# Kernel tuning notes

Measured on AMD Instinct MI355X. Metric: run time of the kernel, lower is better.

## Reference

```python
import jax, jax.numpy as jnp
import numpy as np

H = 16      # num_attention_heads
D = 1024    # hidden_size
DH = D // H # attention_head_size
LN_EPS = 1e-5


def setup_inputs() -> dict:
    key = jax.random.key(0)
    ks = jax.random.split(key, 12)
    B, S = 2, 2048
    s = 0.02
    return {
        "hidden_states": jax.random.normal(ks[0], (B, S, D), jnp.float32),
        "attention_mask": jnp.zeros((B, 1, 1, S), jnp.float32),
        "Wq": jax.random.normal(ks[1], (D, D), jnp.float32) * s,
        "bq": jnp.zeros((D,), jnp.float32),
        "Wk": jax.random.normal(ks[2], (D, D), jnp.float32) * s,
        "bk": jnp.zeros((D,), jnp.float32),
        "Wv": jax.random.normal(ks[3], (D, D), jnp.float32) * s,
        "bv": jnp.zeros((D,), jnp.float32),
        "med_bias": jax.random.normal(ks[4], (H, 1, 1), jnp.float32) * s,
        "Wo": jax.random.normal(ks[5], (D, D), jnp.float32) * s,
        "bo": jnp.zeros((D,), jnp.float32),
        "gamma": jnp.ones((D,), jnp.float32),
        "beta": jnp.zeros((D,), jnp.float32),
    }


def _heads(x):
    # (B,S,D) -> (B,H,S,DH)
    B, S, _ = x.shape
    return x.reshape(B, S, H, DH).transpose(0, 2, 1, 3)


def reference(hidden_states, attention_mask, Wq, bq, Wk, bk, Wv, bv,
              med_bias, Wo, bo, gamma, beta):
    B, S, _ = hidden_states.shape
    q = _heads(hidden_states @ Wq.T + bq)
    k = _heads(hidden_states @ Wk.T + bk)
    v = _heads(hidden_states @ Wv.T + bv)

    scale = 1.0 / jnp.sqrt(jnp.asarray(DH, hidden_states.dtype))
    # scores: (B,H,S,S); per-head medical bias + additive mask
    scores = jnp.einsum('bhqd,bhkd->bhqk', q, k) * scale
    scores = scores + med_bias[None, :, :, :] + attention_mask
    probs = jax.nn.softmax(scores, axis=-1)  # dropout is identity in eval

    ctx = jnp.einsum('bhqk,bhkd->bhqd', probs, v)
    ctx = ctx.transpose(0, 2, 1, 3).reshape(B, S, D)

    attn_out = ctx @ Wo.T + bo
    x = hidden_states + attn_out

    mu = jnp.mean(x, axis=-1, keepdims=True)
    var = jnp.mean(jnp.square(x - mu), axis=-1, keepdims=True)
    return (x - mu) * jax.lax.rsqrt(var + LN_EPS) * gamma + beta
```

## Files before the change

kernel.cpp:

```cpp
#include <hip/hip_runtime.h>
#include <hip/hip_bf16.h>

#define S_LEN 2048
#define NH 16
#define DH 64
#define DMODEL 1024
#define M_TOT 4096
#define LOG2E 1.44269504f

typedef __attribute__((ext_vector_type(8))) short bf16x8;
typedef __attribute__((ext_vector_type(4))) float f32x4;
typedef unsigned short u16;
typedef unsigned short us8 __attribute__((ext_vector_type(8)));

__device__ inline u16 f2bf(float f) {
    union { float f; unsigned u; } c; c.f = f;
    unsigned r = c.u + 0x7fffu + ((c.u >> 16) & 1u);
    return (u16)(r >> 16);
}

__device__ inline void load_lds16(const u16* g, u16* l) {
    __builtin_amdgcn_global_load_lds((const __attribute__((address_space(1))) void*)g,
                                     (__attribute__((address_space(3))) void*)l, 16, 0, 0);
}

__device__ inline us8 pack8(float4 a, float4 b) {
    us8 o;
    o[0] = f2bf(a.x); o[1] = f2bf(a.y); o[2] = f2bf(a.z); o[3] = f2bf(a.w);
    o[4] = f2bf(b.x); o[5] = f2bf(b.y); o[6] = f2bf(b.z); o[7] = f2bf(b.w);
    return o;
}

__global__ __launch_bounds__(256) void conv_bf16(
    const float* __restrict__ src, u16* __restrict__ dst)
{
    const size_t i = ((size_t)blockIdx.x * 256 + threadIdx.x) * 8;
    const float4 a = *(const float4*)(src + i);
    const float4 b = *(const float4*)(src + i + 4);
    *(us8*)(dst + i) = pack8(a, b);
}

__global__ __launch_bounds__(256) void conv4(
    const float* __restrict__ w0, const float* __restrict__ w1,
    const float* __restrict__ w2, const float* __restrict__ w3,
    u16* __restrict__ dst)
{
    const int z = blockIdx.y;
    const float* src = (z == 0) ? w0 : (z == 1) ? w1 : (z == 2) ? w2 : w3;
    const size_t i = ((size_t)blockIdx.x * 256 + threadIdx.x) * 8;
    const float4 a = *(const float4*)(src + i);
    const float4 b = *(const float4*)(src + i + 4);
    *(us8*)(dst + (size_t)z * (DMODEL * DMODEL) + i) = pack8(a, b);
}

__global__ __launch_bounds__(256) void gen_cm(
    const float* __restrict__ mask, float* __restrict__ cm, u16* __restrict__ cmb)
{
    const int i = blockIdx.x * 256 + threadIdx.x;
    const float c = exp2f(mask[i] * LOG2E);
    cm[i] = c;
    cmb[i] = f2bf(c);
}

__global__ __launch_bounds__(256) void gemm_qkv(
    const u16* __restrict__ hsb, const u16* __restrict__ wbf,
    const float* __restrict__ bq, const float* __restrict__ bk, const float* __restrict__ bv,
    const float* __restrict__ cm,
    u16* __restrict__ qb, u16* __restrict__ kb, u16* __restrict__ vT)
{
    __shared__ u16 lA[2][128 * 32];
    __shared__ u16 lB[2][128 * 32];
    const int tid = threadIdx.x, lane = tid & 63, w = tid >> 6;
    const int l15 = lane & 15, lg = lane >> 4;
    const int wr = w >> 1, wc = w & 1;
    const int m0 = blockIdx.y * 128, n0 = blockIdx.x * 128;
    const int z = blockIdx.z;
    const u16* Wp = wbf + (size_t)z * (DMODEL * DMODEL);
    const float* bias = (z == 0) ? bq : (z == 1) ? bk : bv;

    const u16 *aptr[2], *wptr[2]; int adst[2];
#pragma unroll
    for (int i = 0; i < 2; ++i) {
        const int rowb = (w * 2 + i) * 16;
        const int row = rowb + (lane >> 2);
        const int gc = (lane & 3) ^ ((row >> 1) & 3);
        aptr[i] = hsb + (size_t)(m0 + row) * DMODEL + gc * 8;
        wptr[i] = Wp + (size_t)(n0 + row) * DMODEL + gc * 8;
        adst[i] = rowb * 32;
    }
    int afo[4], bfo[4];
#pragma unroll
    for (int i = 0; i < 4; ++i) {
        const int rA = wr * 64 + i * 16 + l15;
        afo[i] = rA * 32 + ((lg ^ ((rA >> 1) & 3)) * 8);
        const int rB = wc * 64 + i * 16 + l15;
        bfo[i] = rB * 32 + ((lg ^ ((rB >> 1) & 3)) * 8);
    }

    f32x4 acc[4][4] = {};

#pragma unroll
    for (int i = 0; i < 2; ++i) {
        load_lds16(aptr[i], &lA[0][adst[i]]);
        load_lds16(wptr[i], &lB[0][adst[i]]);
    }

    int cur = 0;
    for (int t = 0; t < 32; ++t) {
        if (t < 31) {
#pragma unroll
            for (int i = 0; i < 2; ++i) {
                load_lds16(aptr[i] + (t + 1) * 32, &lA[cur ^ 1][adst[i]]);
                load_lds16(wptr[i] + (t + 1) * 32, &lB[cur ^ 1][adst[i]]);
            }
            asm volatile("s_waitcnt vmcnt(4)" ::: "memory");
        } else {
            asm volatile("s_waitcnt vmcnt(0)" ::: "memory");
        }
        __builtin_amdgcn_s_barrier();
        __builtin_amdgcn_sched_barrier(0);

        bf16x8 af[4], bfr[4];
#pragma unroll
        for (int i = 0; i < 4; ++i) {
            af[i] = *(bf16x8*)&lA[cur][afo[i]];
            bfr[i] = *(bf16x8*)&lB[cur][bfo[i]];
        }
        __builtin_amdgcn_s_setprio(1);
#pragma unroll
        for (int i = 0; i < 4; ++i)
#pragma unroll
            for (int j = 0; j < 4; ++j)
                acc[i][j] = __builtin_amdgcn_mfma_f32_16x16x32_bf16(af[i], bfr[j], acc[i][j], 0, 0, 0);
        __builtin_amdgcn_s_setprio(0);
        __builtin_amdgcn_s_barrier();
        cur ^= 1;
    }

    const float qsc = 0.125f * LOG2E;
    float bn[4];
#pragma unroll
    for (int j = 0; j < 4; ++j) bn[j] = bias[n0 + wc * 64 + j * 16 + l15];

#pragma unroll
    for (int i = 0; i < 4; ++i) {
        const int mbase = m0 + wr * 64 + i * 16 + lg * 4;
        if (z == 0) {
#pragma unroll
            for (int j = 0; j < 4; ++j) {
                const int n = n0 + wc * 64 + j * 16 + l15;
#pragma unroll
                for (int e = 0; e < 4; ++e)
                    qb[(size_t)(mbase + e) * DMODEL + n] = f2bf((acc[i][j][e] + bn[j]) * qsc);
            }
        } else if (z == 1) {
#pragma unroll
            for (int j = 0; j < 4; ++j) {
                const int n = n0 + wc * 64 + j * 16 + l15;
#pragma unroll
                for (int e = 0; e < 4; ++e)
                    kb[(size_t)(mbase + e) * DMODEL + n] = f2bf(acc[i][j][e] + bn[j]);
            }
        } else {
            const int bb = mbase >> 11, s = mbase & 2047;
            const float4 c4 = *(const float4*)&cm[bb * S_LEN + s];
#pragma unroll
            for (int j = 0; j < 4; ++j) {
                const int n = n0 + wc * 64 + j * 16 + l15;
                const int hh = n >> 6, dh = n & 63;
                ushort4 uv;
                uv.x = f2bf((acc[i][j][0] + bn[j]) * c4.x);
                uv.y = f2bf((acc[i][j][1] + bn[j]) * c4.y);
                uv.z = f2bf((acc[i][j][2] + bn[j]) * c4.z);
                uv.w = f2bf((acc[i][j][3] + bn[j]) * c4.w);
                *(ushort4*)&vT[((size_t)(bb * NH + hh) * DH + dh) * S_LEN + s] = uv;
            }
        }
    }
}

__global__ __launch_bounds__(256) void gemm_o(
    const u16* __restrict__ ctx, const u16* __restrict__ wobf,
    const float* __restrict__ bo, const float* __restrict__ resid,
    float* __restrict__ X)
{
    __shared__ u16 lA[2][128 * 32];
    __shared__ u16 lB[2][128 * 32];
    const int tid = threadIdx.x, lane = tid & 63, w = tid >> 6;
    const int l15 = lane & 15, lg = lane >> 4;
    const int wr = w >> 1, wc = w & 1;
    const int m0 = blockIdx.y * 128, n0 = blockIdx.x * 128;

    const u16 *aptr[2], *wptr[2]; int adst[2];
#pragma unroll
    for (int i = 0; i < 2; ++i) {
        const int rowb = (w * 2 + i) * 16;
        const int row = rowb + (lane >> 2);
        const int gc = (lane & 3) ^ ((row >> 1) & 3);
        aptr[i] = ctx + (size_t)(m0 + row) * DMODEL + gc * 8;
        wptr[i] = wobf + (size_t)(n0 + row) * DMODEL + gc * 8;
        adst[i] = rowb * 32;
    }
    int afo[4], bfo[4];
#pragma unroll
    for (int i = 0; i < 4; ++i) {
        const int rA = wr * 64 + i * 16 + l15;
        afo[i] = rA * 32 + ((lg ^ ((rA >> 1) & 3)) * 8);
        const int rB = wc * 64 + i * 16 + l15;
        bfo[i] = rB * 32 + ((lg ^ ((rB >> 1) & 3)) * 8);
    }

    f32x4 acc[4][4] = {};

#pragma unroll
    for (int i = 0; i < 2; ++i) {
        load_lds16(aptr[i], &lA[0][adst[i]]);
        load_lds16(wptr[i], &lB[0][adst[i]]);
    }

    int cur = 0;
    for (int t = 0; t < 32; ++t) {
        if (t < 31) {
#pragma unroll
            for (int i = 0; i < 2; ++i) {
                load_lds16(aptr[i] + (t + 1) * 32, &lA[cur ^ 1][adst[i]]);
                load_lds16(wptr[i] + (t + 1) * 32, &lB[cur ^ 1][adst[i]]);
            }
            asm volatile("s_waitcnt vmcnt(4)" ::: "memory");
        } else {
            asm volatile("s_waitcnt vmcnt(0)" ::: "memory");
        }
        __builtin_amdgcn_s_barrier();
        __builtin_amdgcn_sched_barrier(0);

        bf16x8 af[4], bfr[4];
#pragma unroll
        for (int i = 0; i < 4; ++i) {
            af[i] = *(bf16x8*)&lA[cur][afo[i]];
            bfr[i] = *(bf16x8*)&lB[cur][bfo[i]];
        }
        __builtin_amdgcn_s_setprio(1);
#pragma unroll
        for (int i = 0; i < 4; ++i)
#pragma unroll
            for (int j = 0; j < 4; ++j)
                acc[i][j] = __builtin_amdgcn_mfma_f32_16x16x32_bf16(af[i], bfr[j], acc[i][j], 0, 0, 0);
        __builtin_amdgcn_s_setprio(0);
        __builtin_amdgcn_s_barrier();
        cur ^= 1;
    }

#pragma unroll
    for (int i = 0; i < 4; ++i) {
#pragma unroll
        for (int j = 0; j < 4; ++j) {
            const int n = n0 + wc * 64 + j * 16 + l15;
            const float bnj = bo[n];
#pragma unroll
            for (int e = 0; e < 4; ++e) {
                const int m = m0 + wr * 64 + i * 16 + lg * 4 + e;
                X[(size_t)m * DMODEL + n] = acc[i][j][e] + bnj + resid[(size_t)m * DMODEL + n];
            }
        }
    }
}

__global__ __launch_bounds__(512, 4) void attn9(
    const u16* __restrict__ qg, const u16* __restrict__ kg,
    const u16* __restrict__ vTg, const u16* __restrict__ cmb,
    u16* __restrict__ ctx)
{
    __shared__ u16 Kl[2][128 * 64];
    __shared__ u16 Vl[2][64 * 128];
    __shared__ u16 Pl8[8][16 * 64];

    const int tid = threadIdx.x, lane = tid & 63, w = tid >> 6;
    const int bx = blockIdx.x;
    const int x = bx & 7, rest = bx >> 3;
    const int qt = rest & 15, g2 = rest >> 4;
    const int hb = g2 * 8 + x;
    const int h = hb & (NH - 1), b = hb >> 4;

    const int l15 = lane & 15, lg = lane >> 4;
    const int q0 = qt * 128 + w * 16;
    const size_t rowbase = (size_t)b * S_LEN * DMODEL + h * DH;
    const size_t vbase = (size_t)(b * NH + h) * DH * S_LEN;
    u16* Pw = Pl8[w];

    bf16x8 aq[2];
#pragma unroll
    for (int kf = 0; kf < 2; ++kf)
        aq[kf] = *(const bf16x8*)&qg[rowbase + (size_t)(q0 + l15) * DMODEL + kf * 32 + lg * 8];

    const int lx = l15 & 7;
    int kbase[2];
#pragma unroll
    for (int kf = 0; kf < 2; ++kf)
        kbase[kf] = l15 * 64 + (((kf * 4 + lg) ^ lx) * 8);
    int vb2[4];
#pragma unroll
    for (int kf2 = 0; kf2 < 4; ++kf2)
        vb2[kf2] = l15 * 128 + (((kf2 * 4 + lg) ^ lx) * 8);
    const int phi = l15 >> 3, plo = l15 & 7;

    size_t ksoff[2], vsoff[2];
    int ldst[2];
#pragma unroll
    for (int t = 0; t < 2; ++t) {
        const int ck = t * 512 + tid;
        const int krow = ck >> 3, kslot = ck & 7;
        ksoff[t] = (size_t)krow * DMODEL + ((kslot ^ (krow & 7)) * 8);
        const int vrow = ck >> 4, vslot = ck & 15;
        vsoff[t] = (size_t)vrow * S_LEN + ((vslot ^ (vrow & 7)) * 8);
        ldst[t] = (t * 512 + w * 64) * 8;
    }
    const u16* cmb_b = cmb + (size_t)b * S_LEN + lg * 8;

    f32x4 po[4] = {};
    f32x4 pol = {};

    bf16x8 cf[4];
#pragma unroll
    for (int j = 0; j < 4; ++j)
        cf[j] = *(const bf16x8*)&cmb_b[j * 32];
    const u16* kp = kg + rowbase;
    const u16* vp = vTg + vbase;
#pragma unroll
    for (int t = 0; t < 2; ++t) {
        load_lds16(kp + ksoff[t], &Kl[0][ldst[t]]);
        load_lds16(vp + vsoff[t], &Vl[0][ldst[t]]);
    }
    kp += 128 * DMODEL; vp += 128;

    int cur = 0;
    for (int kt = 0; kt < S_LEN / 128; ++kt) {
        bf16x8 nx[4];
        if (kt + 1 < S_LEN / 128) {
#pragma unroll
            for (int j = 0; j < 4; ++j)
                nx[j] = *(const bf16x8*)&cmb_b[(kt + 1) * 128 + j * 32];
#pragma unroll
            for (int t = 0; t < 2; ++t) {
                load_lds16(kp + ksoff[t], &Kl[cur ^ 1][ldst[t]]);
                load_lds16(vp + vsoff[t], &Vl[cur ^ 1][ldst[t]]);
            }
            kp += 128 * DMODEL; vp += 128;
            asm volatile("s_waitcnt vmcnt(8)" ::: "memory");
        } else {
#pragma unroll
            for (int j = 0; j < 4; ++j) nx[j] = cf[j];
            asm volatile("s_waitcnt vmcnt(0)" ::: "memory");
        }
        __builtin_amdgcn_s_barrier();
        __builtin_amdgcn_sched_barrier(0);

#pragma unroll
        for (int h2 = 0; h2 < 2; ++h2) {
            f32x4 sa[4] = {};
            bf16x8 bkf[4][2];
#pragma unroll
            for (int nf = 0; nf < 4; ++nf)
#pragma unroll
                for (int kf = 0; kf < 2; ++kf)
                    bkf[nf][kf] = *(bf16x8*)&Kl[cur][(h2 * 4 + nf) * 1024 + kbase[kf]];
            __builtin_amdgcn_s_setprio(1);
#pragma unroll
            for (int nf = 0; nf < 4; ++nf)
#pragma unroll
                for (int kf = 0; kf < 2; ++kf)
                    sa[nf] = __builtin_amdgcn_mfma_f32_16x16x32_bf16(aq[kf], bkf[nf][kf], sa[nf], 0, 0, 0);
            __builtin_amdgcn_s_setprio(0);

#pragma unroll
            for (int e = 0; e < 4; ++e) {
                const int prow = lg * 4 + e;
                const int pbase = prow * 64 + plo;
                const int pxor = prow & 7;
#pragma unroll
                for (int nf = 0; nf < 4; ++nf) {
                    union { float f; unsigned u; } cv;
                    cv.f = exp2f(sa[nf][e]);
                    Pw[pbase + (((nf * 2 + phi) ^ pxor) * 8)] = (u16)(cv.u >> 16);
                }
            }

#pragma unroll
            for (int j = 0; j < 2; ++j) {
                const int kf2 = h2 * 2 + j;
                bf16x8 ap = *(bf16x8*)&Pw[kbase[j]];
                bf16x8 bv[4];
#pragma unroll
                for (int df = 0; df < 4; ++df)
                    bv[df] = *(bf16x8*)&Vl[cur][df * 2048 + vb2[kf2]];
                const bf16x8 cfk = cf[kf2];
                __builtin_amdgcn_s_setprio(1);
#pragma unroll
                for (int df = 0; df < 4; ++df)
                    po[df] = __builtin_amdgcn_mfma_f32_16x16x32_bf16(ap, bv[df], po[df], 0, 0, 0);
                pol = __builtin_amdgcn_mfma_f32_16x16x32_bf16(ap, cfk, pol, 0, 0, 0);
                __builtin_amdgcn_s_setprio(0);
            }
        }
        __builtin_amdgcn_s_barrier();
#pragma unroll
        for (int j = 0; j < 4; ++j) cf[j] = nx[j];
        cur ^= 1;
    }

#pragma unroll
    for (int e = 0; e < 4; ++e) {
        const float inv = 1.0f / pol[e];
        const int qrow = q0 + lg * 4 + e;
#pragma unroll
        for (int df = 0; df < 4; ++df)
            ctx[((size_t)b * S_LEN + qrow) * DMODEL + h * DH + df * 16 + l15] = f2bf(po[df][e] * inv);
    }
}

__global__ __launch_bounds__(256) void ln_kernel(
    const float* __restrict__ xin, float* __restrict__ y,
    const float* __restrict__ gamma, const float* __restrict__ beta)
{
    const int row = blockIdx.x;
    const int tid = threadIdx.x;
    float4 vv = *(const float4*)(xin + (size_t)row * DMODEL + tid * 4);
    float s = vv.x + vv.y + vv.z + vv.w;
    float s2 = vv.x * vv.x + vv.y * vv.y + vv.z * vv.z + vv.w * vv.w;
#pragma unroll
    for (int d = 1; d < 64; d <<= 1) { s += __shfl_xor(s, d); s2 += __shfl_xor(s2, d); }
    __shared__ float rs[4], rs2[4];
    if ((tid & 63) == 0) { rs[tid >> 6] = s; rs2[tid >> 6] = s2; }
    __syncthreads();
    s = rs[0] + rs[1] + rs[2] + rs[3];
    s2 = rs2[0] + rs2[1] + rs2[2] + rs2[3];
    const float mu = s * (1.f / DMODEL);
    const float var = s2 * (1.f / DMODEL) - mu * mu;
    const float inv = rsqrtf(var + 1e-5f);
    const float4 g = *(const float4*)(gamma + tid * 4);
    const float4 bt = *(const float4*)(beta + tid * 4);
    vv.x = (vv.x - mu) * inv * g.x + bt.x;
    vv.y = (vv.y - mu) * inv * g.y + bt.y;
    vv.z = (vv.z - mu) * inv * g.z + bt.z;
    vv.w = (vv.w - mu) * inv * g.w + bt.w;
    *(float4*)(y + (size_t)row * DMODEL + tid * 4) = vv;
}

extern "C" void kernel_launch(void* const* d_in, const int* in_sizes, int n_in,
                              void* d_out, int out_size, void* d_ws, size_t ws_size,
                              hipStream_t stream) {
    const float* hs    = (const float*)d_in[0];
    const float* mask  = (const float*)d_in[1];
    const float* Wq    = (const float*)d_in[2];
    const float* bq    = (const float*)d_in[3];
    const float* Wk    = (const float*)d_in[4];
    const float* bk    = (const float*)d_in[5];
    const float* Wv    = (const float*)d_in[6];
    const float* bv    = (const float*)d_in[7];
    const float* Wo    = (const float*)d_in[9];
    const float* bo    = (const float*)d_in[10];
    const float* gamma = (const float*)d_in[11];
    const float* beta  = (const float*)d_in[12];
    float* out = (float*)d_out;

    const size_t MN = (size_t)M_TOT * DMODEL;
    const size_t WN = (size_t)DMODEL * DMODEL;
    u16* qb      = (u16*)d_ws;
    u16* kb      = qb + MN;
    u16* vT      = kb + MN;
    u16* scratch = vT + MN;
    float* X     = (float*)d_ws;

    u16*  wbf = (u16*)out;
    float* cm = out + MN - 4096 - 2048;
    u16*  cmb = (u16*)(out + MN - 2048);

    dim3 blk(256);

    conv_bf16<<<MN / 2048, blk, 0, stream>>>(hs, scratch);
    conv4<<<dim3(WN / 2048, 4), blk, 0, stream>>>(Wq, Wk, Wv, Wo, wbf);
    gen_cm<<<(2 * S_LEN) / 256, blk, 0, stream>>>(mask, cm, cmb);
    gemm_qkv<<<dim3(DMODEL / 128, M_TOT / 128, 3), blk, 0, stream>>>(
        scratch, wbf, bq, bk, bv, cm, qb, kb, vT);
    attn9<<<dim3(512), dim3(512), 0, stream>>>(qb, kb, vT, cmb, scratch);
    gemm_o<<<dim3(DMODEL / 128, M_TOT / 128), blk, 0, stream>>>(
        scratch, wbf + 3 * WN, bo, hs, X);
    ln_kernel<<<M_TOT, blk, 0, stream>>>(X, out, gamma, beta);
}
```

Before: 152.9 us.

## Keep attention P in registers via transposed QK MFMA and remap GEMM tiles per XCD

The QK^T MFMA now has its operands swapped, so each lane holds the transposed score layout. The exponentiated probabilities are packed straight into registers as the A operand for the PV MFMA, which removes the per-wave LDS round-trip for P. The V and mask-column reads are reshaped into 4-element pieces to match the new layout. Both GEMMs also remap the flat block index so that blocks landing on the same XCD share neighbouring M/N tiles, aiming for better L2 reuse. The trade-off is more, smaller LDS reads for V and eight register-held mask pieces, and the s_waitcnt vmcnt threshold was raised from 8 to 12 to cover the extra loads.

```diff
diff --git a/kernel.cpp b/kernel.cpp
--- a/kernel.cpp
+++ b/kernel.cpp
@@ -73,8 +73,13 @@
     const int tid = threadIdx.x, lane = tid & 63, w = tid >> 6;
     const int l15 = lane & 15, lg = lane >> 4;
     const int wr = w >> 1, wc = w & 1;
-    const int m0 = blockIdx.y * 128, n0 = blockIdx.x * 128;
-    const int z = blockIdx.z;
+
+    const int flat = blockIdx.x + 8 * (blockIdx.y + 32 * blockIdx.z);
+    const int xcd = flat & 7, l = flat >> 3;
+    const int z = l >> 5, r = l & 31;
+    const int n0 = ((xcd >> 2) * 4 + (r >> 3)) * 128;
+    const int m0 = ((xcd & 3) * 8 + (r & 7)) * 128;
+
     const u16* Wp = wbf + (size_t)z * (DMODEL * DMODEL);
     const float* bias = (z == 0) ? bq : (z == 1) ? bk : bv;
 
@@ -189,7 +194,11 @@
     const int tid = threadIdx.x, lane = tid & 63, w = tid >> 6;
     const int l15 = lane & 15, lg = lane >> 4;
     const int wr = w >> 1, wc = w & 1;
-    const int m0 = blockIdx.y * 128, n0 = blockIdx.x * 128;
+
+    const int flat = blockIdx.x + 8 * blockIdx.y;
+    const int xcd = flat & 7, l = flat >> 3;
+    const int n0 = ((xcd >> 2) * 4 + (l >> 3)) * 128;
+    const int m0 = ((xcd & 3) * 8 + (l & 7)) * 128;
 
     const u16 *aptr[2], *wptr[2]; int adst[2];
 #pragma unroll
@@ -265,14 +274,13 @@
     }
 }
 
-__global__ __launch_bounds__(512, 4) void attn9(
+__global__ __launch_bounds__(512, 4) void attn10(
     const u16* __restrict__ qg, const u16* __restrict__ kg,
     const u16* __restrict__ vTg, const u16* __restrict__ cmb,
     u16* __restrict__ ctx)
 {
     __shared__ u16 Kl[2][128 * 64];
     __shared__ u16 Vl[2][64 * 128];
-    __shared__ u16 Pl8[8][16 * 64];
 
     const int tid = threadIdx.x, lane = tid & 63, w = tid >> 6;
     const int bx = blockIdx.x;
@@ -282,10 +290,10 @@
     const int h = hb & (NH - 1), b = hb >> 4;
 
     const int l15 = lane & 15, lg = lane >> 4;
+    const int lgh = lg >> 1, lgl = lg & 1;
     const int q0 = qt * 128 + w * 16;
     const size_t rowbase = (size_t)b * S_LEN * DMODEL + h * DH;
     const size_t vbase = (size_t)(b * NH + h) * DH * S_LEN;
-    u16* Pw = Pl8[w];
 
     bf16x8 aq[2];
 #pragma unroll
@@ -297,11 +305,11 @@
 #pragma unroll
     for (int kf = 0; kf < 2; ++kf)
         kbase[kf] = l15 * 64 + (((kf * 4 + lg) ^ lx) * 8);
-    int vb2[4];
-#pragma unroll
-    for (int kf2 = 0; kf2 < 4; ++kf2)
-        vb2[kf2] = l15 * 128 + (((kf2 * 4 + lg) ^ lx) * 8);
-    const int phi = l15 >> 3, plo = l15 & 7;
+    int sx[4];
+#pragma unroll
+    for (int n16 = 0; n16 < 4; ++n16)
+        sx[n16] = (((n16 * 2 + lgh) ^ lx) * 8) + lgl * 4;
+    const int vrow0 = l15 * 128;
 
     size_t ksoff[2], vsoff[2];
     int ldst[2];
@@ -314,15 +322,15 @@
         vsoff[t] = (size_t)vrow * S_LEN + ((vslot ^ (vrow & 7)) * 8);
         ldst[t] = (t * 512 + w * 64) * 8;
     }
-    const u16* cmb_b = cmb + (size_t)b * S_LEN + lg * 8;
+    const u16* cmb_c = cmb + (size_t)b * S_LEN + lg * 4;
 
     f32x4 po[4] = {};
     f32x4 pol = {};
 
-    bf16x8 cf[4];
-#pragma unroll
-    for (int j = 0; j < 4; ++j)
-        cf[j] = *(const bf16x8*)&cmb_b[j * 32];
+    uint2 cfd[8];
+#pragma unroll
+    for (int j = 0; j < 8; ++j)
+        cfd[j] = *(const uint2*)&cmb_c[j * 16];
     const u16* kp = kg + rowbase;
     const u16* vp = vTg + vbase;
 #pragma unroll
@@ -334,21 +342,21 @@
 
     int cur = 0;
     for (int kt = 0; kt < S_LEN / 128; ++kt) {
-        bf16x8 nx[4];
+        uint2 nx[8];
         if (kt + 1 < S_LEN / 128) {
 #pragma unroll
-            for (int j = 0; j < 4; ++j)
-                nx[j] = *(const bf16x8*)&cmb_b[(kt + 1) * 128 + j * 32];
+            for (int j = 0; j < 8; ++j)
+                nx[j] = *(const uint2*)&cmb_c[(kt + 1) * 128 + j * 16];
 #pragma unroll
             for (int t = 0; t < 2; ++t) {
                 load_lds16(kp + ksoff[t], &Kl[cur ^ 1][ldst[t]]);
                 load_lds16(vp + vsoff[t], &Vl[cur ^ 1][ldst[t]]);
             }
             kp += 128 * DMODEL; vp += 128;
-            asm volatile("s_waitcnt vmcnt(8)" ::: "memory");
+            asm volatile("s_waitcnt vmcnt(12)" ::: "memory");
         } else {
 #pragma unroll
-            for (int j = 0; j < 4; ++j) nx[j] = cf[j];
+            for (int j = 0; j < 8; ++j) nx[j] = cfd[j];
             asm volatile("s_waitcnt vmcnt(0)" ::: "memory");
         }
         __builtin_amdgcn_s_barrier();
@@ -368,42 +376,46 @@
             for (int nf = 0; nf < 4; ++nf)
 #pragma unroll
                 for (int kf = 0; kf < 2; ++kf)
-                    sa[nf] = __builtin_amdgcn_mfma_f32_16x16x32_bf16(aq[kf], bkf[nf][kf], sa[nf], 0, 0, 0);
+                    sa[nf] = __builtin_amdgcn_mfma_f32_16x16x32_bf16(bkf[nf][kf], aq[kf], sa[nf], 0, 0, 0);
             __builtin_amdgcn_s_setprio(0);
 
-#pragma unroll
-            for (int e = 0; e < 4; ++e) {
-                const int prow = lg * 4 + e;
-                const int pbase = prow * 64 + plo;
-                const int pxor = prow & 7;
-#pragma unroll
-                for (int nf = 0; nf < 4; ++nf) {
-                    union { float f; unsigned u; } cv;
-                    cv.f = exp2f(sa[nf][e]);
-                    Pw[pbase + (((nf * 2 + phi) ^ pxor) * 8)] = (u16)(cv.u >> 16);
+            unsigned pk[4][2];
+#pragma unroll
+            for (int nf = 0; nf < 4; ++nf) {
+                union { float f; unsigned u; } c0, c1, c2, c3;
+                c0.f = exp2f(sa[nf][0]); c1.f = exp2f(sa[nf][1]);
+                c2.f = exp2f(sa[nf][2]); c3.f = exp2f(sa[nf][3]);
+                pk[nf][0] = (c0.u >> 16) | (c1.u & 0xFFFF0000u);
+                pk[nf][1] = (c2.u >> 16) | (c3.u & 0xFFFF0000u);
+            }
+
+#pragma unroll
+            for (int jb = 0; jb < 2; ++jb) {
+                union { bf16x8 v; unsigned u[4]; } ap;
+                ap.u[0] = pk[2 * jb][0];     ap.u[1] = pk[2 * jb][1];
+                ap.u[2] = pk[2 * jb + 1][0]; ap.u[3] = pk[2 * jb + 1][1];
+                union { bf16x8 v; uint2 d[2]; } cfr;
+                cfr.d[0] = cfd[h2 * 4 + 2 * jb];
+                cfr.d[1] = cfd[h2 * 4 + 2 * jb + 1];
+                bf16x8 bv[4];
+#pragma unroll
+                for (int df = 0; df < 4; ++df) {
+                    union { bf16x8 v; ushort4 s[2]; } t;
+                    t.s[0] = *(ushort4*)&Vl[cur][vrow0 + df * 2048 + h2 * 64 + sx[2 * jb]];
+                    t.s[1] = *(ushort4*)&Vl[cur][vrow0 + df * 2048 + h2 * 64 + sx[2 * jb + 1]];
+                    bv[df] = t.v;
                 }
-            }
-
-#pragma unroll
-            for (int j = 0; j < 2; ++j) {
-                const int kf2 = h2 * 2 + j;
-                bf16x8 ap = *(bf16x8*)&Pw[kbase[j]];
-                bf16x8 bv[4];
+                __builtin_amdgcn_s_setprio(1);
 #pragma unroll
                 for (int df = 0; df < 4; ++df)
-                    bv[df] = *(bf16x8*)&Vl[cur][df * 2048 + vb2[kf2]];
-                const bf16x8 cfk = cf[kf2];
-                __builtin_amdgcn_s_setprio(1);
-#pragma unroll
-                for (int df = 0; df < 4; ++df)
-                    po[df] = __builtin_amdgcn_mfma_f32_16x16x32_bf16(ap, bv[df], po[df], 0, 0, 0);
-                pol = __builtin_amdgcn_mfma_f32_16x16x32_bf16(ap, cfk, pol, 0, 0, 0);
+                    po[df] = __builtin_amdgcn_mfma_f32_16x16x32_bf16(ap.v, bv[df], po[df], 0, 0, 0);
+                pol = __builtin_amdgcn_mfma_f32_16x16x32_bf16(ap.v, cfr.v, pol, 0, 0, 0);
                 __builtin_amdgcn_s_setprio(0);
             }
         }
         __builtin_amdgcn_s_barrier();
 #pragma unroll
-        for (int j = 0; j < 4; ++j) cf[j] = nx[j];
+        for (int j = 0; j < 8; ++j) cfd[j] = nx[j];
         cur ^= 1;
     }
 
@@ -479,10 +491,10 @@
     conv_bf16<<<MN / 2048, blk, 0, stream>>>(hs, scratch);
     conv4<<<dim3(WN / 2048, 4), blk, 0, stream>>>(Wq, Wk, Wv, Wo, wbf);
     gen_cm<<<(2 * S_LEN) / 256, blk, 0, stream>>>(mask, cm, cmb);
-    gemm_qkv<<<dim3(DMODEL / 128, M_TOT / 128, 3), blk, 0, stream>>>(
+    gemm_qkv<<<dim3(8, 32, 3), blk, 0, stream>>>(
         scratch, wbf, bq, bk, bv, cm, qb, kb, vT);
-    attn9<<<dim3(512), dim3(512), 0, stream>>>(qb, kb, vT, cmb, scratch);
-    gemm_o<<<dim3(DMODEL / 128, M_TOT / 128), blk, 0, stream>>>(
+    attn10<<<dim3(512), dim3(512), 0, stream>>>(qb, kb, vT, cmb, scratch);
+    gemm_o<<<dim3(8, 32), blk, 0, stream>>>(
         scratch, wbf + 3 * WN, bo, hs, X);
     ln_kernel<<<M_TOT, blk, 0, stream>>>(X, out, gamma, beta);
 }
```

Result: no change. 154.9 us (+1.3%).
